# Performance work log

Measured on AMD Instinct MI355X. Metric: run time of the kernel, lower is better.

The kernel has to match this reference:

```python
import jax, jax.numpy as jnp
import numpy as np

DIM = 2048
N_HEADS = 16
HEAD_DIM = DIM // N_HEADS  # 128
MAX_LEN = 2048
B, T = 2, 2048
RESTORE_SCALE = DIM ** 0.5  # sqkinit / sqkscale = 1 / (1/sqrt(dim))
SQK_SCALE = 1.0 / DIM ** 0.5


def _rope_tables(seq_len, head_dim, dtype=jnp.float32):
    d2 = head_dim // 2
    pos = jnp.arange(seq_len, dtype=dtype)                     # [T]
    theta = 1.0 / (10000.0 ** (jnp.arange(0, head_dim, 2, dtype=dtype) / head_dim))  # [d2]
    ang = pos[:, None] * theta[None, :]                        # [T, d2]
    return jnp.cos(ang), jnp.sin(ang)


def _apply_rope(x, cos, sin):
    # x: [B, H, T, D]; cos/sin: [T, D/2] broadcast over B,H
    d2 = x.shape[-1] // 2
    xr, xi = x[..., :d2], x[..., d2:]
    return jnp.concatenate([xr * cos - xi * sin, xr * sin + xi * cos], axis=-1)


def setup_inputs() -> dict:
    key = jax.random.key(0)
    ks = jax.random.split(key, 5)
    s = 0.02
    return {
        "x":  jax.random.normal(ks[0], (B, T, DIM), jnp.float32),
        "Wq": jax.random.normal(ks[1], (DIM, DIM), jnp.float32) * s,
        "Wk": jax.random.normal(ks[2], (DIM, DIM), jnp.float32) * s,
        "Wv": jax.random.normal(ks[3], (DIM, DIM), jnp.float32) * s,
        "Wo": jax.random.normal(ks[4], (DIM, DIM), jnp.float32) * s,
        "sqk": jnp.ones((N_HEADS, 1, HEAD_DIM), jnp.float32) * SQK_SCALE,
    }


def reference(x, Wq, Wk, Wv, Wo, sqk):
    Bc, Tc, C = x.shape
    # QKV projections (torch Linear: x @ W.T), split heads -> [B, H, T, D]
    def proj(W):
        return (x @ W.T).reshape(Bc, Tc, N_HEADS, HEAD_DIM).transpose(0, 2, 1, 3)
    q, k, v = proj(Wq), proj(Wk), proj(Wv)

    cos, sin = _rope_tables(Tc, HEAD_DIM, x.dtype)
    actual_sqk = sqk * RESTORE_SCALE  # [H, 1, D]
    q = _apply_rope(q, cos, sin) * actual_sqk
    k = _apply_rope(k, cos, sin) * actual_sqk

    # SDPA with scale = sqrt(head_dim) (as in the source, not 1/sqrt)
    scale = HEAD_DIM ** 0.5
    scores = jnp.einsum("bhtd,bhsd->bhts", q, k) * scale  # [B, H, T, T]
    causal = jnp.tril(jnp.ones((Tc, Tc), bool))
    scores = jnp.where(causal, scores, -jnp.inf)
    attn = jax.nn.softmax(scores, axis=-1)
    out = jnp.einsum("bhts,bhsd->bhtd", attn, v)           # [B, H, T, D]
    out = out.transpose(0, 2, 1, 3).reshape(Bc, Tc, C)

    y = out @ Wo.T
    # F.normalize(p=2, dim=-1, eps=1e-12)
    norm = jnp.linalg.norm(y, axis=-1, keepdims=True)
    return y / jnp.maximum(norm, 1e-12)
```

## Files before the change

kernel.cpp:

```cpp
#include <hip/hip_runtime.h>

#define DEVFN __device__ __forceinline__

typedef float    floatx4 __attribute__((ext_vector_type(4)));
typedef _Float16 half8   __attribute__((ext_vector_type(8)));
typedef _Float16 half4v  __attribute__((ext_vector_type(4)));

#define MFMA16H(a, b, c) __builtin_amdgcn_mfma_f32_16x16x32_f16((a), (b), (c), 0, 0, 0)

DEVFN void async16(void* lds, const void* g) {
  __builtin_amdgcn_global_load_lds(
      (const __attribute__((address_space(1))) unsigned int*)g,
      (__attribute__((address_space(3))) unsigned int*)lds, 16, 0, 0);
}
DEVFN half8 ld8h(const _Float16* p) { return *(const half8*)p; }

__global__ __launch_bounds__(256) void cvt_prep(
    const float4* __restrict__ x, const float4* __restrict__ wq,
    const float4* __restrict__ wk, const float4* __restrict__ wv,
    const float4* __restrict__ wo,
    half4v* __restrict__ xh, half4v* __restrict__ xl,
    half4v* __restrict__ qo, half4v* __restrict__ ko,
    half4v* __restrict__ vo, half4v* __restrict__ oo,
    float* __restrict__ cosT, float* __restrict__ sinT) {
  int i = blockIdx.x * 256 + threadIdx.x;
  {
    float4 v = x[i];
    half4v h = {(_Float16)v.x, (_Float16)v.y, (_Float16)v.z, (_Float16)v.w};
    half4v l = {(_Float16)(v.x - (float)h.x), (_Float16)(v.y - (float)h.y),
                (_Float16)(v.z - (float)h.z), (_Float16)(v.w - (float)h.w)};
    xh[i] = h;
    xl[i] = l;
  }
  if (i < 1048576) {
    float4 v = wq[i];
    qo[i] = (half4v){(_Float16)v.x, (_Float16)v.y, (_Float16)v.z, (_Float16)v.w};
    v = wk[i];
    ko[i] = (half4v){(_Float16)v.x, (_Float16)v.y, (_Float16)v.z, (_Float16)v.w};
    v = wv[i];
    vo[i] = (half4v){(_Float16)v.x, (_Float16)v.y, (_Float16)v.z, (_Float16)v.w};
    v = wo[i];
    oo[i] = (half4v){(_Float16)v.x, (_Float16)v.y, (_Float16)v.z, (_Float16)v.w};
  }
  if (i < 131072) {
    int t = i >> 6, d = i & 63;
    double theta = exp(-((double)(2 * d) / 128.0) * log(10000.0));
    double ang = (double)t * theta;
    cosT[i] = (float)cos(ang);
    sinT[i] = (float)sin(ang);
  }
}

__global__ __launch_bounds__(256, 2) void gemm_qkv_f16(
    const _Float16* __restrict__ xhp, const _Float16* __restrict__ xlp,
    const _Float16* __restrict__ wq, const _Float16* __restrict__ wk,
    const _Float16* __restrict__ wv,
    const float* __restrict__ cosT, const float* __restrict__ sinT,
    const float* __restrict__ sqk,
    _Float16* __restrict__ qhi, _Float16* __restrict__ qlo,
    _Float16* __restrict__ khi, _Float16* __restrict__ vo) {
  constexpr int Kd = 2048;
  const int n0 = blockIdx.x * 128, m0 = blockIdx.y * 128;
  const int tid = threadIdx.x, w = tid >> 6, lane = tid & 63;
  const int quad = lane >> 4, l16 = lane & 15;

  __shared__ __align__(16) _Float16 smem[5 * 4096];
  _Float16* Xh = smem;
  _Float16* Xl = smem + 4096;
  _Float16* Qs = smem + 8192;
  _Float16* Ks = smem + 12288;
  _Float16* Vs = smem + 16384;
  _Float16* stH = smem + w * 2176;
  _Float16* stL = smem + 8704 + w * 2176;

  floatx4 accQ[2][8], accK[2][8], accV[2][8];
#pragma unroll
  for (int i = 0; i < 2; i++)
#pragma unroll
    for (int j = 0; j < 8; j++) {
      accQ[i][j] = (floatx4){0.f, 0.f, 0.f, 0.f};
      accK[i][j] = (floatx4){0.f, 0.f, 0.f, 0.f};
      accV[i][j] = (floatx4){0.f, 0.f, 0.f, 0.f};
    }

  const int t0 = 2 * w, t1 = 2 * w + 1;
  const size_t xo0 = (size_t)(m0 + t0 * 16 + l16) * Kd + quad * 8;
  const size_t xo1 = (size_t)(m0 + t1 * 16 + l16) * Kd + quad * 8;
  const size_t wo0 = (size_t)(n0 + t0 * 16 + l16) * Kd + quad * 8;
  const size_t wo1 = (size_t)(n0 + t1 * 16 + l16) * Kd + quad * 8;

  for (int k0 = 0; k0 < Kd; k0 += 32) {
    __syncthreads();
    async16(&Xh[t0 * 512], xhp + xo0 + k0);
    async16(&Xh[t1 * 512], xhp + xo1 + k0);
    async16(&Xl[t0 * 512], xlp + xo0 + k0);
    async16(&Xl[t1 * 512], xlp + xo1 + k0);
    async16(&Qs[t0 * 512], wq + wo0 + k0);
    async16(&Qs[t1 * 512], wq + wo1 + k0);
    async16(&Ks[t0 * 512], wk + wo0 + k0);
    async16(&Ks[t1 * 512], wk + wo1 + k0);
    async16(&Vs[t0 * 512], wv + wo0 + k0);
    async16(&Vs[t1 * 512], wv + wo1 + k0);
    __syncthreads();
    half8 ah0 = ld8h(&Xh[t0 * 512 + lane * 8]);
    half8 ah1 = ld8h(&Xh[t1 * 512 + lane * 8]);
    half8 al0 = ld8h(&Xl[t0 * 512 + lane * 8]);
    half8 al1 = ld8h(&Xl[t1 * 512 + lane * 8]);
#pragma unroll
    for (int j = 0; j < 8; j++) {
      half8 b;
      b = ld8h(&Qs[j * 512 + lane * 8]);
      accQ[0][j] = MFMA16H(ah0, b, accQ[0][j]);
      accQ[1][j] = MFMA16H(ah1, b, accQ[1][j]);
      accQ[0][j] = MFMA16H(al0, b, accQ[0][j]);
      accQ[1][j] = MFMA16H(al1, b, accQ[1][j]);
      b = ld8h(&Ks[j * 512 + lane * 8]);
      accK[0][j] = MFMA16H(ah0, b, accK[0][j]);
      accK[1][j] = MFMA16H(ah1, b, accK[1][j]);
      accK[0][j] = MFMA16H(al0, b, accK[0][j]);
      accK[1][j] = MFMA16H(al1, b, accK[1][j]);
      b = ld8h(&Vs[j * 512 + lane * 8]);
      accV[0][j] = MFMA16H(ah0, b, accV[0][j]);
      accV[1][j] = MFMA16H(ah1, b, accV[1][j]);
    }
  }

  __syncthreads();

  const int h = n0 >> 7;
#pragma unroll
  for (int i = 0; i < 2; i++) {
    const int grow0 = m0 + (2 * w + i) * 16;
    const int bb = grow0 >> 11, tt0 = grow0 & 2047;
    const size_t gbase = (((size_t)(bb * 16 + h)) * 2048 + tt0) * 128;

#pragma unroll
    for (int j = 0; j < 4; j++) {
      int d = j * 16 + l16;
      float s1 = sqk[h * 128 + d] * 512.0f;
      float s2 = sqk[h * 128 + d + 64] * 512.0f;
#pragma unroll
      for (int r = 0; r < 4; r++) {
        int t = tt0 + quad * 4 + r;
        float c = cosT[t * 64 + d], s = sinT[t * 64 + d];
        float xr = accQ[i][j][r], xi = accQ[i][j + 4][r];
        float o1 = (xr * c - xi * s) * s1;
        float o2 = (xr * s + xi * c) * s2;
        _Float16 h1 = (_Float16)o1, h2 = (_Float16)o2;
        int rl = quad * 4 + r;
        stH[rl * 136 + d] = h1;
        stH[rl * 136 + d + 64] = h2;
        stL[rl * 136 + d] = (_Float16)(o1 - (float)h1);
        stL[rl * 136 + d + 64] = (_Float16)(o2 - (float)h2);
      }
    }
#pragma unroll
    for (int it = 0; it < 4; it++) {
      int pb = it * 1024 + lane * 16;
      int rr = pb >> 8, cs = (pb & 255) >> 1;
      *(half8*)(qhi + gbase + rr * 128 + cs) = ld8h(&stH[rr * 136 + cs]);
      *(half8*)(qlo + gbase + rr * 128 + cs) = ld8h(&stL[rr * 136 + cs]);
    }

#pragma unroll
    for (int j = 0; j < 4; j++) {
      int d = j * 16 + l16;
      float s1 = sqk[h * 128 + d] * 45.254834f;
      float s2 = sqk[h * 128 + d + 64] * 45.254834f;
#pragma unroll
      for (int r = 0; r < 4; r++) {
        int t = tt0 + quad * 4 + r;
        float c = cosT[t * 64 + d], s = sinT[t * 64 + d];
        float xr = accK[i][j][r], xi = accK[i][j + 4][r];
        int rl = quad * 4 + r;
        stH[rl * 136 + d] = (_Float16)((xr * c - xi * s) * s1);
        stH[rl * 136 + d + 64] = (_Float16)((xr * s + xi * c) * s2);
      }
    }
#pragma unroll
    for (int it = 0; it < 4; it++) {
      int pb = it * 1024 + lane * 16;
      int rr = pb >> 8, cs = (pb & 255) >> 1;
      *(half8*)(khi + gbase + rr * 128 + cs) = ld8h(&stH[rr * 136 + cs]);
    }

#pragma unroll
    for (int j = 0; j < 8; j++)
#pragma unroll
      for (int r = 0; r < 4; r++)
        stH[(quad * 4 + r) * 136 + j * 16 + l16] = (_Float16)accV[i][j][r];
#pragma unroll
    for (int it = 0; it < 4; it++) {
      int pb = it * 1024 + lane * 16;
      int rr = pb >> 8, cs = (pb & 255) >> 1;
      *(half8*)(vo + gbase + rr * 128 + cs) = ld8h(&stH[rr * 136 + cs]);
    }
  }
}

__global__ __launch_bounds__(256) void transpose_v(
    const unsigned short* __restrict__ v, unsigned short* __restrict__ vt) {
  __shared__ unsigned short tile[32][33];
  int t0 = blockIdx.x * 32, d0 = blockIdx.y * 32, bh = blockIdx.z;
  int tx = threadIdx.x & 31, ty = threadIdx.x >> 5;
  for (int r = ty; r < 32; r += 8)
    tile[r][tx] = v[((size_t)bh * 2048 + t0 + r) * 128 + d0 + tx];
  __syncthreads();
  for (int r = ty; r < 32; r += 8)
    vt[((size_t)bh * 128 + d0 + r) * 2048 + t0 + tx] = tile[tx][r];
}

__global__ __launch_bounds__(256, 2) void flash_attn(
    const _Float16* __restrict__ qhp, const _Float16* __restrict__ qlp,
    const _Float16* __restrict__ khp,
    const _Float16* __restrict__ vtp, _Float16* __restrict__ aout) {
  constexpr int T = 2048, HD = 128;
  const int bh = blockIdx.x, qt = blockIdx.y;
  const int q0 = qt * 128;
  const int tid = threadIdx.x, w = tid >> 6, lane = tid & 63;
  const int quad = lane >> 4, l16 = lane & 15;

  __shared__ __align__(16) _Float16 Kh[8192];
  __shared__ __align__(16) _Float16 Vt[8192];
  __shared__ __align__(16) _Float16 Pb[4][16 * 72];

  const size_t qkbase = (size_t)bh * T * HD;

  half8 qh[2][4], ql[2][4];
#pragma unroll
  for (int i = 0; i < 2; i++)
#pragma unroll
    for (int s = 0; s < 4; s++) {
      size_t off = qkbase + (size_t)(q0 + w * 32 + i * 16 + l16) * HD + s * 32 + quad * 8;
      qh[i][s] = *(const half8*)(qhp + off);
      ql[i][s] = *(const half8*)(qlp + off);
    }

  floatx4 o[2][8];
#pragma unroll
  for (int i = 0; i < 2; i++)
#pragma unroll
    for (int dt = 0; dt < 8; dt++) o[i][dt] = (floatx4){0.f, 0.f, 0.f, 0.f};
  float mrow[2][4], lrow[2][4];
#pragma unroll
  for (int i = 0; i < 2; i++)
#pragma unroll
    for (int r = 0; r < 4; r++) { mrow[i][r] = -3e38f; lrow[i][r] = 0.f; }

  const int ntiles = q0 / 64 + 2;
  for (int kt = 0; kt < ntiles; ++kt) {
    const int s0 = kt * 64;
    __syncthreads();
    for (int c = w; c < 16; c += 4) {
      int tt = c >> 2, ss = c & 3;
      size_t go = qkbase + (size_t)(s0 + tt * 16 + l16) * HD + ss * 32 + quad * 8;
      async16(&Kh[c * 512], khp + go);
      int dt = c >> 1, vs = c & 1;
      size_t vo = (size_t)bh * HD * T + (size_t)(dt * 16 + l16) * T + s0 + vs * 32 + quad * 8;
      async16(&Vt[c * 512], vtp + vo);
    }
    __syncthreads();

    floatx4 S[2][4];
#pragma unroll
    for (int i = 0; i < 2; i++)
#pragma unroll
      for (int j = 0; j < 4; j++) S[i][j] = (floatx4){0.f, 0.f, 0.f, 0.f};

#pragma unroll
    for (int s = 0; s < 4; s++) {
#pragma unroll
      for (int j = 0; j < 4; j++) {
        half8 kh = ld8h(&Kh[(j * 4 + s) * 512 + lane * 8]);
        S[0][j] = MFMA16H(qh[0][s], kh, S[0][j]);
        S[1][j] = MFMA16H(qh[1][s], kh, S[1][j]);
        S[0][j] = MFMA16H(ql[0][s], kh, S[0][j]);
        S[1][j] = MFMA16H(ql[1][s], kh, S[1][j]);
      }
    }

    if (s0 + 63 > q0) {
#pragma unroll
      for (int i = 0; i < 2; i++) {
        int rb = q0 + w * 32 + i * 16 + quad * 4;
#pragma unroll
        for (int j = 0; j < 4; j++) {
          int cg = s0 + j * 16 + l16;
#pragma unroll
          for (int r = 0; r < 4; r++)
            if (cg > rb + r) S[i][j][r] = -3e38f;
        }
      }
    }

    half8 pf[2][2];
#pragma unroll
    for (int i = 0; i < 2; i++) {
#pragma unroll
      for (int r = 0; r < 4; r++) {
        float mx = fmaxf(fmaxf(S[i][0][r], S[i][1][r]), fmaxf(S[i][2][r], S[i][3][r]));
#pragma unroll
        for (int d = 1; d < 16; d <<= 1) mx = fmaxf(mx, __shfl_xor(mx, d, 64));
        float mnew = fmaxf(mrow[i][r], mx);
        float al = __expf(mrow[i][r] - mnew);
        mrow[i][r] = mnew;
        float sum = 0.f;
#pragma unroll
        for (int j = 0; j < 4; j++) {
          float p = __expf(S[i][j][r] - mnew);
          S[i][j][r] = p;
          sum += p;
        }
#pragma unroll
        for (int d = 1; d < 16; d <<= 1) sum += __shfl_xor(sum, d, 64);
        lrow[i][r] = lrow[i][r] * al + sum;
#pragma unroll
        for (int dt = 0; dt < 8; dt++) o[i][dt][r] *= al;
      }
#pragma unroll
      for (int r = 0; r < 4; r++)
#pragma unroll
        for (int j = 0; j < 4; j++)
          Pb[w][(quad * 4 + r) * 72 + j * 16 + l16] = (_Float16)S[i][j][r];
      pf[i][0] = ld8h(&Pb[w][l16 * 72 + quad * 8]);
      pf[i][1] = ld8h(&Pb[w][l16 * 72 + 32 + quad * 8]);
    }

#pragma unroll
    for (int dt = 0; dt < 8; dt++) {
#pragma unroll
      for (int s = 0; s < 2; s++) {
        half8 vf = ld8h(&Vt[(dt * 2 + s) * 512 + lane * 8]);
        o[0][dt] = MFMA16H(pf[0][s], vf, o[0][dt]);
        o[1][dt] = MFMA16H(pf[1][s], vf, o[1][dt]);
      }
    }
  }

  const int b = bh >> 4, h = bh & 15;
#pragma unroll
  for (int i = 0; i < 2; i++) {
#pragma unroll
    for (int r = 0; r < 4; r++) {
      int trow = q0 + w * 32 + i * 16 + quad * 4 + r;
      float linv = 1.0f / lrow[i][r];
      size_t base = ((size_t)(b * T + trow)) * 2048 + h * 128;
#pragma unroll
      for (int dt = 0; dt < 8; dt++)
        aout[base + dt * 16 + l16] = (_Float16)(o[i][dt][r] * linv);
    }
  }
}

__global__ __launch_bounds__(256, 2) void gemm_o_f16(
    const _Float16* __restrict__ A, const _Float16* __restrict__ B,
    float* __restrict__ outF) {
  constexpr int Kd = 2048;
  constexpr int Nd = 2048;
  const int n0 = blockIdx.x * 128, m0 = blockIdx.y * 128;
  const int tid = threadIdx.x, w = tid >> 6, lane = tid & 63;
  const int quad = lane >> 4, l16 = lane & 15;

  __shared__ __align__(16) _Float16 As[8192];
  __shared__ __align__(16) _Float16 Bs[8192];

  floatx4 acc[2][8];
#pragma unroll
  for (int i = 0; i < 2; i++)
#pragma unroll
    for (int j = 0; j < 8; j++) acc[i][j] = (floatx4){0.f, 0.f, 0.f, 0.f};

  const int t0 = 2 * w, t1 = 2 * w + 1;
  const size_t ao0 = (size_t)(m0 + t0 * 16 + l16) * Kd + quad * 8;
  const size_t ao1 = (size_t)(m0 + t1 * 16 + l16) * Kd + quad * 8;
  const size_t bo0 = (size_t)(n0 + t0 * 16 + l16) * Kd + quad * 8;
  const size_t bo1 = (size_t)(n0 + t1 * 16 + l16) * Kd + quad * 8;

  for (int k0 = 0; k0 < Kd; k0 += 64) {
    __syncthreads();
    async16(&As[t0 * 512], A + ao0 + k0);
    async16(&As[t1 * 512], A + ao1 + k0);
    async16(&As[4096 + t0 * 512], A + ao0 + k0 + 32);
    async16(&As[4096 + t1 * 512], A + ao1 + k0 + 32);
    async16(&Bs[t0 * 512], B + bo0 + k0);
    async16(&Bs[t1 * 512], B + bo1 + k0);
    async16(&Bs[4096 + t0 * 512], B + bo0 + k0 + 32);
    async16(&Bs[4096 + t1 * 512], B + bo1 + k0 + 32);
    __syncthreads();
    half8 a00 = ld8h(&As[t0 * 512 + lane * 8]);
    half8 a10 = ld8h(&As[t1 * 512 + lane * 8]);
    half8 a01 = ld8h(&As[4096 + t0 * 512 + lane * 8]);
    half8 a11 = ld8h(&As[4096 + t1 * 512 + lane * 8]);
#pragma unroll
    for (int j = 0; j < 8; j++) {
      half8 b0 = ld8h(&Bs[j * 512 + lane * 8]);
      acc[0][j] = MFMA16H(a00, b0, acc[0][j]);
      acc[1][j] = MFMA16H(a10, b0, acc[1][j]);
      half8 b1 = ld8h(&Bs[4096 + j * 512 + lane * 8]);
      acc[0][j] = MFMA16H(a01, b1, acc[0][j]);
      acc[1][j] = MFMA16H(a11, b1, acc[1][j]);
    }
  }

#pragma unroll
  for (int i = 0; i < 2; i++) {
    int rbase = m0 + (2 * w + i) * 16 + quad * 4;
#pragma unroll
    for (int j = 0; j < 8; j++) {
      int col = n0 + j * 16 + l16;
#pragma unroll
      for (int r = 0; r < 4; r++)
        outF[(size_t)(rbase + r) * Nd + col] = acc[i][j][r];
    }
  }
}

__global__ __launch_bounds__(256) void rownorm(const float* __restrict__ y,
                                               float* __restrict__ out) {
  int row = blockIdx.x;
  const float4* yr = (const float4*)(y + (size_t)row * 2048);
  float4* od = (float4*)(out + (size_t)row * 2048);
  int t = threadIdx.x;
  float4 v0 = yr[t], v1 = yr[t + 256];
  float ss = v0.x * v0.x + v0.y * v0.y + v0.z * v0.z + v0.w * v0.w +
             v1.x * v1.x + v1.y * v1.y + v1.z * v1.z + v1.w * v1.w;
#pragma unroll
  for (int d = 1; d < 64; d <<= 1) ss += __shfl_xor(ss, d, 64);
  __shared__ float red[4];
  if ((t & 63) == 0) red[t >> 6] = ss;
  __syncthreads();
  float tot = red[0] + red[1] + red[2] + red[3];
  float inv = 1.0f / fmaxf(sqrtf(tot), 1e-12f);
  v0.x *= inv; v0.y *= inv; v0.z *= inv; v0.w *= inv;
  v1.x *= inv; v1.y *= inv; v1.z *= inv; v1.w *= inv;
  od[t] = v0;
  od[t + 256] = v1;
}

extern "C" void kernel_launch(void* const* d_in, const int* in_sizes, int n_in,
                              void* d_out, int out_size, void* d_ws, size_t ws_size,
                              hipStream_t stream) {
  (void)in_sizes; (void)n_in; (void)out_size; (void)ws_size;
  const float* x   = (const float*)d_in[0];
  const float* Wq  = (const float*)d_in[1];
  const float* Wk  = (const float*)d_in[2];
  const float* Wv  = (const float*)d_in[3];
  const float* Wo  = (const float*)d_in[4];
  const float* sqk = (const float*)d_in[5];
  char* ws = (char*)d_ws;

  constexpr size_t SZX = 8388608ull * 2;
  constexpr size_t SZW = 4194304ull * 2;

  size_t o_xh = 0;
  size_t o_xl = o_xh + SZX;
  size_t o_wq = o_xl + SZX;
  size_t o_wk = o_wq + SZW;
  size_t o_wv = o_wk + SZW;
  size_t o_wo = o_wv + SZW;
  size_t o_qh = o_wo + SZW;
  size_t o_ql = o_qh + SZX;
  size_t o_kh = o_ql + SZX;
  size_t o_v  = o_kh + SZX;
  size_t o_vt = o_v + SZX;
  size_t o_cos = o_vt + SZX;
  size_t o_sin = o_cos + 2048 * 64 * 4;
  size_t o_aout = o_wq;
  size_t o_y    = o_qh;

  _Float16* xh = (_Float16*)(ws + o_xh);
  _Float16* xl = (_Float16*)(ws + o_xl);
  _Float16* wq = (_Float16*)(ws + o_wq);
  _Float16* wk = (_Float16*)(ws + o_wk);
  _Float16* wv = (_Float16*)(ws + o_wv);
  _Float16* wo = (_Float16*)(ws + o_wo);
  _Float16* qh = (_Float16*)(ws + o_qh);
  _Float16* ql = (_Float16*)(ws + o_ql);
  _Float16* kh = (_Float16*)(ws + o_kh);
  _Float16* v  = (_Float16*)(ws + o_v);
  _Float16* vt = (_Float16*)(ws + o_vt);
  float* cosT = (float*)(ws + o_cos);
  float* sinT = (float*)(ws + o_sin);
  _Float16* aout = (_Float16*)(ws + o_aout);
  float* y = (float*)(ws + o_y);

  cvt_prep<<<8192, 256, 0, stream>>>((const float4*)x, (const float4*)Wq,
                                     (const float4*)Wk, (const float4*)Wv,
                                     (const float4*)Wo, (half4v*)xh, (half4v*)xl,
                                     (half4v*)wq, (half4v*)wk, (half4v*)wv,
                                     (half4v*)wo, cosT, sinT);

  gemm_qkv_f16<<<dim3(16, 32), 256, 0, stream>>>(xh, xl, wq, wk, wv, cosT,
                                                 sinT, sqk, qh, ql, kh, v);
  transpose_v<<<dim3(64, 4, 32), 256, 0, stream>>>((const unsigned short*)v,
                                                   (unsigned short*)vt);

  flash_attn<<<dim3(32, 16), 256, 0, stream>>>(qh, ql, kh, vt, aout);

  gemm_o_f16<<<dim3(16, 32), 256, 0, stream>>>(aout, wo, y);
  rownorm<<<4096, 256, 0, stream>>>(y, (float*)d_out);
}
```

Measured before the change: 531.5 us.

## Split QKV GEMM into pipelined QK and V kernels, fuse V transpose, double-buffer attention

Replaces the single QKV projection kernel with two 512-thread kernels on 256x128 tiles. Both use multi-stage LDS buffering (double-buffered X, triple-buffered weights) with explicit waitcnt, barriers and setprio to overlap global loads with MFMA work. The V kernel writes its output already transposed, removing the separate transpose kernel and its round trip through memory. Flash attention now double-buffers the K/V tiles, prefetching the next tile while computing the current one, at the cost of twice the LDS and possibly lower occupancy.

```diff
diff --git a/kernel.cpp b/kernel.cpp
--- a/kernel.cpp
+++ b/kernel.cpp
@@ -51,163 +51,288 @@
   }
 }
 
-__global__ __launch_bounds__(256, 2) void gemm_qkv_f16(
+__global__ __launch_bounds__(512, 2) void gemm_qk_f16(
     const _Float16* __restrict__ xhp, const _Float16* __restrict__ xlp,
-    const _Float16* __restrict__ wq, const _Float16* __restrict__ wk,
-    const _Float16* __restrict__ wv,
+    const _Float16* __restrict__ wqp, const _Float16* __restrict__ wkp,
     const float* __restrict__ cosT, const float* __restrict__ sinT,
     const float* __restrict__ sqk,
     _Float16* __restrict__ qhi, _Float16* __restrict__ qlo,
-    _Float16* __restrict__ khi, _Float16* __restrict__ vo) {
-  constexpr int Kd = 2048;
-  const int n0 = blockIdx.x * 128, m0 = blockIdx.y * 128;
+    _Float16* __restrict__ khi) {
+  constexpr int Kd = 2048, NT = 64;
+  const int n0 = blockIdx.x * 128, m0 = blockIdx.y * 256;
   const int tid = threadIdx.x, w = tid >> 6, lane = tid & 63;
   const int quad = lane >> 4, l16 = lane & 15;
-
-  __shared__ __align__(16) _Float16 smem[5 * 4096];
-  _Float16* Xh = smem;
-  _Float16* Xl = smem + 4096;
-  _Float16* Qs = smem + 8192;
-  _Float16* Ks = smem + 12288;
-  _Float16* Vs = smem + 16384;
-  _Float16* stH = smem + w * 2176;
-  _Float16* stL = smem + 8704 + w * 2176;
-
-  floatx4 accQ[2][8], accK[2][8], accV[2][8];
-#pragma unroll
-  for (int i = 0; i < 2; i++)
-#pragma unroll
-    for (int j = 0; j < 8; j++) {
-      accQ[i][j] = (floatx4){0.f, 0.f, 0.f, 0.f};
-      accK[i][j] = (floatx4){0.f, 0.f, 0.f, 0.f};
-      accV[i][j] = (floatx4){0.f, 0.f, 0.f, 0.f};
-    }
-
-  const int t0 = 2 * w, t1 = 2 * w + 1;
-  const size_t xo0 = (size_t)(m0 + t0 * 16 + l16) * Kd + quad * 8;
-  const size_t xo1 = (size_t)(m0 + t1 * 16 + l16) * Kd + quad * 8;
-  const size_t wo0 = (size_t)(n0 + t0 * 16 + l16) * Kd + quad * 8;
-  const size_t wo1 = (size_t)(n0 + t1 * 16 + l16) * Kd + quad * 8;
-
-  for (int k0 = 0; k0 < Kd; k0 += 32) {
-    __syncthreads();
-    async16(&Xh[t0 * 512], xhp + xo0 + k0);
-    async16(&Xh[t1 * 512], xhp + xo1 + k0);
-    async16(&Xl[t0 * 512], xlp + xo0 + k0);
-    async16(&Xl[t1 * 512], xlp + xo1 + k0);
-    async16(&Qs[t0 * 512], wq + wo0 + k0);
-    async16(&Qs[t1 * 512], wq + wo1 + k0);
-    async16(&Ks[t0 * 512], wk + wo0 + k0);
-    async16(&Ks[t1 * 512], wk + wo1 + k0);
-    async16(&Vs[t0 * 512], wv + wo0 + k0);
-    async16(&Vs[t1 * 512], wv + wo1 + k0);
-    __syncthreads();
-    half8 ah0 = ld8h(&Xh[t0 * 512 + lane * 8]);
-    half8 ah1 = ld8h(&Xh[t1 * 512 + lane * 8]);
-    half8 al0 = ld8h(&Xl[t0 * 512 + lane * 8]);
-    half8 al1 = ld8h(&Xl[t1 * 512 + lane * 8]);
-#pragma unroll
-    for (int j = 0; j < 8; j++) {
-      half8 b;
-      b = ld8h(&Qs[j * 512 + lane * 8]);
-      accQ[0][j] = MFMA16H(ah0, b, accQ[0][j]);
-      accQ[1][j] = MFMA16H(ah1, b, accQ[1][j]);
-      accQ[0][j] = MFMA16H(al0, b, accQ[0][j]);
-      accQ[1][j] = MFMA16H(al1, b, accQ[1][j]);
-      b = ld8h(&Ks[j * 512 + lane * 8]);
-      accK[0][j] = MFMA16H(ah0, b, accK[0][j]);
-      accK[1][j] = MFMA16H(ah1, b, accK[1][j]);
-      accK[0][j] = MFMA16H(al0, b, accK[0][j]);
-      accK[1][j] = MFMA16H(al1, b, accK[1][j]);
-      b = ld8h(&Vs[j * 512 + lane * 8]);
-      accV[0][j] = MFMA16H(ah0, b, accV[0][j]);
-      accV[1][j] = MFMA16H(ah1, b, accV[1][j]);
-    }
-  }
-
-  __syncthreads();
+  const int c0 = w & 1, rb = w >> 1, rgb = rb * 4;
+  const int cgr0 = 2 * c0, cgr1 = 2 * c0 + 1, cgr2 = 2 * c0 + 4, cgr3 = 2 * c0 + 5;
+
+  __shared__ __align__(16) _Float16 smem[57344];
+  _Float16* XH = smem;
+  _Float16* XL = smem + 16384;
+  _Float16* WQ = smem + 32768;
+  _Float16* WK = smem + 45056;
+
+  floatx4 accQ[4][4], accK[4][4];
+#pragma unroll
+  for (int i = 0; i < 4; i++)
+#pragma unroll
+    for (int c = 0; c < 4; c++) {
+      accQ[i][c] = (floatx4){0.f, 0.f, 0.f, 0.f};
+      accK[i][c] = (floatx4){0.f, 0.f, 0.f, 0.f};
+    }
+
+  const size_t xg0 = (size_t)(m0 + 32 * w + l16) * Kd + quad * 8;
+  const size_t xg1 = xg0 + (size_t)16 * Kd;
+  const size_t wg = (size_t)(n0 + 16 * w + l16) * Kd + quad * 8;
+
+#define STAGE_X(T)                                                      \
+  {                                                                     \
+    const int kk_ = (T) * 32;                                           \
+    _Float16* bx_ = XH + ((T) & 1) * 8192;                              \
+    _Float16* bl_ = XL + ((T) & 1) * 8192;                              \
+    async16(bx_ + (2 * w) * 512, xhp + xg0 + kk_);                      \
+    async16(bx_ + (2 * w + 1) * 512, xhp + xg1 + kk_);                  \
+    async16(bl_ + (2 * w) * 512, xlp + xg0 + kk_);                      \
+    async16(bl_ + (2 * w + 1) * 512, xlp + xg1 + kk_);                  \
+  }
+#define STAGE_W(T)                                                      \
+  {                                                                     \
+    const int kk_ = (T) * 32;                                           \
+    async16(WQ + ((T) % 3) * 4096 + w * 512, wqp + wg + kk_);           \
+    async16(WK + ((T) % 3) * 4096 + w * 512, wkp + wg + kk_);           \
+  }
+
+  STAGE_X(0);
+  STAGE_W(0);
+  STAGE_W(1);
+  asm volatile("s_waitcnt vmcnt(2)" ::: "memory");
+  __builtin_amdgcn_s_barrier();
+
+#pragma unroll 1
+  for (int t = 0; t < NT; ++t) {
+    const _Float16* XH_ = XH + (t & 1) * 8192;
+    const _Float16* XL_ = XL + (t & 1) * 8192;
+    const _Float16* WQ_ = WQ + (t % 3) * 4096;
+    const _Float16* WK_ = WK + (t % 3) * 4096;
+
+    half8 ah[4], al[4], bq[4];
+#pragma unroll
+    for (int i = 0; i < 4; i++) {
+      ah[i] = ld8h(XH_ + (rgb + i) * 512 + lane * 8);
+      al[i] = ld8h(XL_ + (rgb + i) * 512 + lane * 8);
+    }
+    bq[0] = ld8h(WQ_ + cgr0 * 512 + lane * 8);
+    bq[1] = ld8h(WQ_ + cgr1 * 512 + lane * 8);
+    bq[2] = ld8h(WQ_ + cgr2 * 512 + lane * 8);
+    bq[3] = ld8h(WQ_ + cgr3 * 512 + lane * 8);
+    if (t + 1 < NT) STAGE_X(t + 1);
+    __builtin_amdgcn_s_barrier();
+    asm volatile("s_waitcnt lgkmcnt(0)");
+    __builtin_amdgcn_sched_barrier(0);
+    __builtin_amdgcn_s_setprio(1);
+#pragma unroll
+    for (int i = 0; i < 4; i++)
+#pragma unroll
+      for (int c = 0; c < 4; c++)
+        accQ[i][c] = MFMA16H(ah[i], bq[c], accQ[i][c]);
+#pragma unroll
+    for (int i = 0; i < 4; i++)
+#pragma unroll
+      for (int c = 0; c < 4; c++)
+        accQ[i][c] = MFMA16H(al[i], bq[c], accQ[i][c]);
+    __builtin_amdgcn_s_setprio(0);
+    __builtin_amdgcn_s_barrier();
+
+    half8 bk[4];
+    bk[0] = ld8h(WK_ + cgr0 * 512 + lane * 8);
+    bk[1] = ld8h(WK_ + cgr1 * 512 + lane * 8);
+    bk[2] = ld8h(WK_ + cgr2 * 512 + lane * 8);
+    bk[3] = ld8h(WK_ + cgr3 * 512 + lane * 8);
+    if (t + 2 < NT) STAGE_W(t + 2);
+    __builtin_amdgcn_s_barrier();
+    asm volatile("s_waitcnt lgkmcnt(0)");
+    __builtin_amdgcn_sched_barrier(0);
+    __builtin_amdgcn_s_setprio(1);
+#pragma unroll
+    for (int i = 0; i < 4; i++)
+#pragma unroll
+      for (int c = 0; c < 4; c++)
+        accK[i][c] = MFMA16H(ah[i], bk[c], accK[i][c]);
+#pragma unroll
+    for (int i = 0; i < 4; i++)
+#pragma unroll
+      for (int c = 0; c < 4; c++)
+        accK[i][c] = MFMA16H(al[i], bk[c], accK[i][c]);
+    __builtin_amdgcn_s_setprio(0);
+
+    if (t + 2 < NT) {
+      asm volatile("s_waitcnt vmcnt(2)" ::: "memory");
+    } else {
+      asm volatile("s_waitcnt vmcnt(0)" ::: "memory");
+    }
+    __builtin_amdgcn_s_barrier();
+  }
+#undef STAGE_X
+#undef STAGE_W
+
+  _Float16* stH = smem + w * 1152;
+  _Float16* stL = smem + 9216 + w * 1152;
 
   const int h = n0 >> 7;
-#pragma unroll
-  for (int i = 0; i < 2; i++) {
-    const int grow0 = m0 + (2 * w + i) * 16;
-    const int bb = grow0 >> 11, tt0 = grow0 & 2047;
-    const size_t gbase = (((size_t)(bb * 16 + h)) * 2048 + tt0) * 128;
-
-#pragma unroll
-    for (int j = 0; j < 4; j++) {
-      int d = j * 16 + l16;
+  const int b = m0 >> 11;
+
+#pragma unroll
+  for (int rg = 0; rg < 4; rg++) {
+    const int tt0 = (m0 & 2047) + rb * 64 + rg * 16;
+    const size_t gbase = (((size_t)(b * 16 + h)) * 2048 + tt0) * 128;
+
+#pragma unroll
+    for (int cj = 0; cj < 2; cj++) {
+      int d = c0 * 32 + cj * 16 + l16;
       float s1 = sqk[h * 128 + d] * 512.0f;
       float s2 = sqk[h * 128 + d + 64] * 512.0f;
 #pragma unroll
       for (int r = 0; r < 4; r++) {
-        int t = tt0 + quad * 4 + r;
-        float c = cosT[t * 64 + d], s = sinT[t * 64 + d];
-        float xr = accQ[i][j][r], xi = accQ[i][j + 4][r];
-        float o1 = (xr * c - xi * s) * s1;
-        float o2 = (xr * s + xi * c) * s2;
+        int tq = tt0 + quad * 4 + r;
+        float cc = cosT[tq * 64 + d], sn = sinT[tq * 64 + d];
+        float xr = accQ[rg][cj][r], xi = accQ[rg][cj + 2][r];
+        float o1 = (xr * cc - xi * sn) * s1;
+        float o2 = (xr * sn + xi * cc) * s2;
         _Float16 h1 = (_Float16)o1, h2 = (_Float16)o2;
         int rl = quad * 4 + r;
-        stH[rl * 136 + d] = h1;
-        stH[rl * 136 + d + 64] = h2;
-        stL[rl * 136 + d] = (_Float16)(o1 - (float)h1);
-        stL[rl * 136 + d + 64] = (_Float16)(o2 - (float)h2);
+        stH[rl * 72 + cj * 16 + l16] = h1;
+        stH[rl * 72 + 32 + cj * 16 + l16] = h2;
+        stL[rl * 72 + cj * 16 + l16] = (_Float16)(o1 - (float)h1);
+        stL[rl * 72 + 32 + cj * 16 + l16] = (_Float16)(o2 - (float)h2);
       }
     }
 #pragma unroll
-    for (int it = 0; it < 4; it++) {
-      int pb = it * 1024 + lane * 16;
-      int rr = pb >> 8, cs = (pb & 255) >> 1;
-      *(half8*)(qhi + gbase + rr * 128 + cs) = ld8h(&stH[rr * 136 + cs]);
-      *(half8*)(qlo + gbase + rr * 128 + cs) = ld8h(&stL[rr * 136 + cs]);
-    }
-
-#pragma unroll
-    for (int j = 0; j < 4; j++) {
-      int d = j * 16 + l16;
+    for (int it = 0; it < 2; it++) {
+      int row = it * 8 + (lane >> 3), pc = (lane & 7) * 8;
+      int d = (pc < 32) ? (c0 * 32 + pc) : (64 + c0 * 32 + (pc - 32));
+      size_t ga = gbase + (size_t)row * 128 + d;
+      *(half8*)(qhi + ga) = ld8h(&stH[row * 72 + pc]);
+      *(half8*)(qlo + ga) = ld8h(&stL[row * 72 + pc]);
+    }
+
+#pragma unroll
+    for (int cj = 0; cj < 2; cj++) {
+      int d = c0 * 32 + cj * 16 + l16;
       float s1 = sqk[h * 128 + d] * 45.254834f;
       float s2 = sqk[h * 128 + d + 64] * 45.254834f;
 #pragma unroll
       for (int r = 0; r < 4; r++) {
-        int t = tt0 + quad * 4 + r;
-        float c = cosT[t * 64 + d], s = sinT[t * 64 + d];
-        float xr = accK[i][j][r], xi = accK[i][j + 4][r];
+        int tq = tt0 + quad * 4 + r;
+        float cc = cosT[tq * 64 + d], sn = sinT[tq * 64 + d];
+        float xr = accK[rg][cj][r], xi = accK[rg][cj + 2][r];
         int rl = quad * 4 + r;
-        stH[rl * 136 + d] = (_Float16)((xr * c - xi * s) * s1);
-        stH[rl * 136 + d + 64] = (_Float16)((xr * s + xi * c) * s2);
+        stH[rl * 72 + cj * 16 + l16] = (_Float16)((xr * cc - xi * sn) * s1);
+        stH[rl * 72 + 32 + cj * 16 + l16] = (_Float16)((xr * sn + xi * cc) * s2);
       }
     }
 #pragma unroll
-    for (int it = 0; it < 4; it++) {
-      int pb = it * 1024 + lane * 16;
-      int rr = pb >> 8, cs = (pb & 255) >> 1;
-      *(half8*)(khi + gbase + rr * 128 + cs) = ld8h(&stH[rr * 136 + cs]);
-    }
-
-#pragma unroll
-    for (int j = 0; j < 8; j++)
+    for (int it = 0; it < 2; it++) {
+      int row = it * 8 + (lane >> 3), pc = (lane & 7) * 8;
+      int d = (pc < 32) ? (c0 * 32 + pc) : (64 + c0 * 32 + (pc - 32));
+      *(half8*)(khi + gbase + (size_t)row * 128 + d) = ld8h(&stH[row * 72 + pc]);
+    }
+  }
+}
+
+__global__ __launch_bounds__(512, 2) void gemm_v_f16(
+    const _Float16* __restrict__ xhp, const _Float16* __restrict__ wvp,
+    _Float16* __restrict__ vt) {
+  constexpr int Kd = 2048, NT = 64;
+  const int n0 = blockIdx.x * 128, m0 = blockIdx.y * 256;
+  const int tid = threadIdx.x, w = tid >> 6, lane = tid & 63;
+  const int quad = lane >> 4, l16 = lane & 15;
+  const int c0 = w & 1, rb = w >> 1, rgb = rb * 4;
+
+  __shared__ __align__(16) _Float16 smem[28672];
+  _Float16* XH = smem;
+  _Float16* WV = smem + 16384;
+
+  floatx4 accV[4][4];
+#pragma unroll
+  for (int i = 0; i < 4; i++)
+#pragma unroll
+    for (int c = 0; c < 4; c++) accV[i][c] = (floatx4){0.f, 0.f, 0.f, 0.f};
+
+  const size_t xg0 = (size_t)(m0 + 32 * w + l16) * Kd + quad * 8;
+  const size_t xg1 = xg0 + (size_t)16 * Kd;
+  const size_t wg = (size_t)(n0 + 16 * w + l16) * Kd + quad * 8;
+
+#define STAGE_XV(T)                                                     \
+  {                                                                     \
+    const int kk_ = (T) * 32;                                           \
+    _Float16* bx_ = XH + ((T) & 1) * 8192;                              \
+    async16(bx_ + (2 * w) * 512, xhp + xg0 + kk_);                      \
+    async16(bx_ + (2 * w + 1) * 512, xhp + xg1 + kk_);                  \
+  }
+#define STAGE_WV(T)                                                     \
+  { async16(WV + ((T) % 3) * 4096 + w * 512, wvp + wg + (T) * 32); }
+
+  STAGE_XV(0);
+  STAGE_WV(0);
+  STAGE_WV(1);
+  asm volatile("s_waitcnt vmcnt(1)" ::: "memory");
+  __builtin_amdgcn_s_barrier();
+
+#pragma unroll 1
+  for (int t = 0; t < NT; ++t) {
+    const _Float16* XH_ = XH + (t & 1) * 8192;
+    const _Float16* WV_ = WV + (t % 3) * 4096;
+
+    half8 ah[4], bv[4];
+#pragma unroll
+    for (int i = 0; i < 4; i++)
+      ah[i] = ld8h(XH_ + (rgb + i) * 512 + lane * 8);
+#pragma unroll
+    for (int c = 0; c < 4; c++)
+      bv[c] = ld8h(WV_ + (4 * c0 + c) * 512 + lane * 8);
+    if (t + 1 < NT) STAGE_XV(t + 1);
+    if (t + 2 < NT) STAGE_WV(t + 2);
+    __builtin_amdgcn_s_barrier();
+    asm volatile("s_waitcnt lgkmcnt(0)");
+    __builtin_amdgcn_sched_barrier(0);
+    __builtin_amdgcn_s_setprio(1);
+#pragma unroll
+    for (int i = 0; i < 4; i++)
+#pragma unroll
+      for (int c = 0; c < 4; c++)
+        accV[i][c] = MFMA16H(ah[i], bv[c], accV[i][c]);
+    __builtin_amdgcn_s_setprio(0);
+    if (t + 2 < NT) {
+      asm volatile("s_waitcnt vmcnt(1)" ::: "memory");
+    } else {
+      asm volatile("s_waitcnt vmcnt(0)" ::: "memory");
+    }
+    __builtin_amdgcn_s_barrier();
+  }
+#undef STAGE_XV
+#undef STAGE_WV
+
+  _Float16* stV = smem + w * 1024;
+
+  const int h = n0 >> 7;
+  const int b = m0 >> 11;
+  const int bh = b * 16 + h;
+
+#pragma unroll
+  for (int rg = 0; rg < 4; rg++) {
+    const int tt0 = (m0 & 2047) + rb * 64 + rg * 16;
+#pragma unroll
+    for (int c = 0; c < 4; c++)
 #pragma unroll
       for (int r = 0; r < 4; r++)
-        stH[(quad * 4 + r) * 136 + j * 16 + l16] = (_Float16)accV[i][j][r];
-#pragma unroll
-    for (int it = 0; it < 4; it++) {
-      int pb = it * 1024 + lane * 16;
-      int rr = pb >> 8, cs = (pb & 255) >> 1;
-      *(half8*)(vo + gbase + rr * 128 + cs) = ld8h(&stH[rr * 136 + cs]);
-    }
-  }
-}
-
-__global__ __launch_bounds__(256) void transpose_v(
-    const unsigned short* __restrict__ v, unsigned short* __restrict__ vt) {
-  __shared__ unsigned short tile[32][33];
-  int t0 = blockIdx.x * 32, d0 = blockIdx.y * 32, bh = blockIdx.z;
-  int tx = threadIdx.x & 31, ty = threadIdx.x >> 5;
-  for (int r = ty; r < 32; r += 8)
-    tile[r][tx] = v[((size_t)bh * 2048 + t0 + r) * 128 + d0 + tx];
-  __syncthreads();
-  for (int r = ty; r < 32; r += 8)
-    vt[((size_t)bh * 128 + d0 + r) * 2048 + t0 + tx] = tile[tx][r];
+        stV[(c * 16 + l16) * 16 + quad * 4 + r] = (_Float16)accV[rg][c][r];
+#pragma unroll
+    for (int it = 0; it < 2; it++) {
+      int dl = it * 32 + (lane >> 1), th = (lane & 1) * 8;
+      int dh = c0 * 64 + dl;
+      size_t ga = ((size_t)bh * 128 + dh) * 2048 + tt0 + th;
+      *(half8*)(vt + ga) = ld8h(&stV[dl * 16 + th]);
+    }
+  }
 }
 
 __global__ __launch_bounds__(256, 2) void flash_attn(
@@ -220,8 +345,8 @@
   const int tid = threadIdx.x, w = tid >> 6, lane = tid & 63;
   const int quad = lane >> 4, l16 = lane & 15;
 
-  __shared__ __align__(16) _Float16 Kh[8192];
-  __shared__ __align__(16) _Float16 Vt[8192];
+  __shared__ __align__(16) _Float16 Kh[2][8192];
+  __shared__ __align__(16) _Float16 Vt[2][8192];
   __shared__ __align__(16) _Float16 Pb[4][16 * 72];
 
   const size_t qkbase = (size_t)bh * T * HD;
@@ -248,18 +373,26 @@
     for (int r = 0; r < 4; r++) { mrow[i][r] = -3e38f; lrow[i][r] = 0.f; }
 
   const int ntiles = q0 / 64 + 2;
-  for (int kt = 0; kt < ntiles; ++kt) {
+
+  auto stageKV = [&](int kt, int set) {
     const int s0 = kt * 64;
-    __syncthreads();
     for (int c = w; c < 16; c += 4) {
       int tt = c >> 2, ss = c & 3;
       size_t go = qkbase + (size_t)(s0 + tt * 16 + l16) * HD + ss * 32 + quad * 8;
-      async16(&Kh[c * 512], khp + go);
+      async16(&Kh[set][c * 512], khp + go);
       int dt = c >> 1, vs = c & 1;
       size_t vo = (size_t)bh * HD * T + (size_t)(dt * 16 + l16) * T + s0 + vs * 32 + quad * 8;
-      async16(&Vt[c * 512], vtp + vo);
-    }
-    __syncthreads();
+      async16(&Vt[set][c * 512], vtp + vo);
+    }
+  };
+
+  stageKV(0, 0);
+  __syncthreads();
+
+  for (int kt = 0; kt < ntiles; ++kt) {
+    const int s0 = kt * 64;
+    const int set = kt & 1;
+    if (kt + 1 < ntiles) stageKV(kt + 1, set ^ 1);
 
     floatx4 S[2][4];
 #pragma unroll
@@ -271,7 +404,7 @@
     for (int s = 0; s < 4; s++) {
 #pragma unroll
       for (int j = 0; j < 4; j++) {
-        half8 kh = ld8h(&Kh[(j * 4 + s) * 512 + lane * 8]);
+        half8 kh = ld8h(&Kh[set][(j * 4 + s) * 512 + lane * 8]);
         S[0][j] = MFMA16H(qh[0][s], kh, S[0][j]);
         S[1][j] = MFMA16H(qh[1][s], kh, S[1][j]);
         S[0][j] = MFMA16H(ql[0][s], kh, S[0][j]);
@@ -330,11 +463,12 @@
     for (int dt = 0; dt < 8; dt++) {
 #pragma unroll
       for (int s = 0; s < 2; s++) {
-        half8 vf = ld8h(&Vt[(dt * 2 + s) * 512 + lane * 8]);
+        half8 vf = ld8h(&Vt[set][(dt * 2 + s) * 512 + lane * 8]);
         o[0][dt] = MFMA16H(pf[0][s], vf, o[0][dt]);
         o[1][dt] = MFMA16H(pf[1][s], vf, o[1][dt]);
       }
     }
+    __syncthreads();
   }
 
   const int b = bh >> 4, h = bh & 15;
@@ -477,7 +611,6 @@
   _Float16* qh = (_Float16*)(ws + o_qh);
   _Float16* ql = (_Float16*)(ws + o_ql);
   _Float16* kh = (_Float16*)(ws + o_kh);
-  _Float16* v  = (_Float16*)(ws + o_v);
   _Float16* vt = (_Float16*)(ws + o_vt);
   float* cosT = (float*)(ws + o_cos);
   float* sinT = (float*)(ws + o_sin);
@@ -490,10 +623,9 @@
                                      (half4v*)wq, (half4v*)wk, (half4v*)wv,
                                      (half4v*)wo, cosT, sinT);
 
-  gemm_qkv_f16<<<dim3(16, 32), 256, 0, stream>>>(xh, xl, wq, wk, wv, cosT,
-                                                 sinT, sqk, qh, ql, kh, v);
-  transpose_v<<<dim3(64, 4, 32), 256, 0, stream>>>((const unsigned short*)v,
-                                                   (unsigned short*)vt);
+  gemm_qk_f16<<<dim3(16, 16), 512, 0, stream>>>(xh, xl, wq, wk, cosT, sinT,
+                                                sqk, qh, ql, kh);
+  gemm_v_f16<<<dim3(16, 16), 512, 0, stream>>>(xh, wv, vt);
 
   flash_attn<<<dim3(32, 16), 256, 0, stream>>>(qh, ql, kh, vt, aout);
 
```

New measurement: 534.3 us. About the same (+0.5%).
